# Kernel optimization log

Measured on AMD Instinct MI355X. Metric: run time of the kernel, lower is better.

The kernel has to match this reference:

```python
import jax, jax.numpy as jnp
import numpy as np

NUM_NODES = 100000
NUM_EDGES = 400000
F_IN = 16          # num_node_features
F_EDGE = 8         # num_edge_features
EMB = 16           # emb_size
NUM_GRAPHS = 256


def setup_inputs() -> dict:
    key = jax.random.key(0)
    ks = jax.random.split(key, 12)
    x = jax.random.normal(ks[0], (NUM_NODES, F_IN), dtype=jnp.float32)
    edge_index = jax.random.randint(ks[1], (2, NUM_EDGES), 0, NUM_NODES, dtype=jnp.int32)
    edge_attr = jax.random.normal(ks[2], (NUM_EDGES, F_EDGE), dtype=jnp.float32)
    batch = jnp.sort(jax.random.randint(ks[3], (NUM_NODES,), 0, NUM_GRAPHS, dtype=jnp.int32))
    s = 0.1
    # edge-network MLP: Linear(F_EDGE -> F_IN*EMB) + ReLU (torch Linear convention: W[out,in])
    nn1_w = jax.random.normal(ks[4], (F_IN * EMB, F_EDGE), dtype=jnp.float32) * s
    nn1_b = jax.random.normal(ks[5], (F_IN * EMB,), dtype=jnp.float32) * s
    # NNConv root weight (bias=False Linear) + separate bias
    root_w = jax.random.normal(ks[6], (EMB, F_IN), dtype=jnp.float32) * s
    conv_b = jax.random.normal(ks[7], (EMB,), dtype=jnp.float32) * s
    lin1_w = jax.random.normal(ks[8], (EMB, 2 * EMB), dtype=jnp.float32) * s
    lin1_b = jax.random.normal(ks[9], (EMB,), dtype=jnp.float32) * s
    lin2_w = jax.random.normal(ks[10], (1, EMB), dtype=jnp.float32) * s
    lin2_b = jax.random.normal(ks[11], (1,), dtype=jnp.float32) * s
    return {"x": x, "edge_index": edge_index, "edge_attr": edge_attr, "batch": batch,
            "nn1_w": nn1_w, "nn1_b": nn1_b, "root_w": root_w, "conv_b": conv_b,
            "lin1_w": lin1_w, "lin1_b": lin1_b, "lin2_w": lin2_w, "lin2_b": lin2_b}


def reference(x, edge_index, edge_attr, batch, nn1_w, nn1_b, root_w, conv_b,
              lin1_w, lin1_b, lin2_w, lin2_b):
    N = x.shape[0]
    src, dst = edge_index[0], edge_index[1]  # PyG: message flows src(j) -> dst(i)
    # edge network -> per-edge weight matrices [E, F_IN, EMB]
    w = jax.nn.relu(edge_attr @ nn1_w.T + nn1_b).reshape(-1, F_IN, EMB)
    # gather source features, per-edge matmul
    msg = jnp.einsum('ei,eio->eo', x[src], w)  # [E, EMB]
    # scatter-mean into target nodes
    sums = jax.ops.segment_sum(msg, dst, num_segments=N)
    cnt = jax.ops.segment_sum(jnp.ones((msg.shape[0],), msg.dtype), dst, num_segments=N)
    agg = sums / jnp.maximum(cnt, 1.0)[:, None]
    # NNConv: root transform + aggregated messages + bias, then outer ReLU
    h = jax.nn.relu(agg + x @ root_w.T + conv_b)  # [N, EMB]
    # global max pool and global mean pool per graph
    gmax = jax.ops.segment_max(h, batch, num_segments=NUM_GRAPHS)
    gsum = jax.ops.segment_sum(h, batch, num_segments=NUM_GRAPHS)
    gcnt = jax.ops.segment_sum(jnp.ones((N,), h.dtype), batch, num_segments=NUM_GRAPHS)
    gmean = gsum / jnp.maximum(gcnt, 1.0)[:, None]
    pooled = jnp.concatenate([gmax, gmean], axis=1)  # [G, 2*EMB]
    h2 = jax.nn.relu(pooled @ lin1_w.T + lin1_b)
    out = h2 @ lin2_w.T + lin2_b  # [G, 1]
    return out
```

## Files before the change

kernel.cpp:

```cpp
#include <hip/hip_runtime.h>

#define NUM_NODES 100000
#define NUM_EDGES 400000
#define F_IN 16
#define F_EDGE 8
#define EMB 16
#define NUM_GRAPHS 256

#define EDGE_TILES 5
#define EDGE_BLOCKS (NUM_EDGES / (32 * EDGE_TILES))

#define NPB 128
#define NODE_BLOCKS ((NUM_NODES + NPB - 1) / NPB)

#define WS_ZERO_FLOATS (NUM_NODES * EMB + NUM_NODES + 2 * NUM_GRAPHS * EMB + NUM_GRAPHS)

__global__ __launch_bounds__(256) void zero_kernel(float4* __restrict__ ws)
{
    const int n4 = WS_ZERO_FLOATS / 4;
    const int stride = gridDim.x * 256;
    for (int i = blockIdx.x * 256 + threadIdx.x; i < n4; i += stride)
        ws[i] = make_float4(0.f, 0.f, 0.f, 0.f);
}

__global__ __launch_bounds__(256) void edge_kernel(
    const float* __restrict__ x, const int* __restrict__ ei,
    const float* __restrict__ ea, const float* __restrict__ nn1_w,
    const float* __restrict__ nn1_b, float* __restrict__ sums,
    float* __restrict__ cnt)
{
    __shared__ float wtp[256 * 12];

    const int tid = threadIdx.x;
    const int eL  = tid >> 4;
    const int o   = tid & 15;

    #pragma unroll
    for (int t = tid; t < F_IN * EMB * F_EDGE; t += 256)
        wtp[(t >> 3) * 12 + (t & 7)] = nn1_w[t];
    wtp[tid * 12 + 8] = nn1_b[tid];
    __syncthreads();

    float br[F_IN];
    #pragma unroll
    for (int i = 0; i < F_IN; i++) br[i] = wtp[(i * 16 + o) * 12 + 8];

    for (int t = 0; t < EDGE_TILES; t++) {
        const int e0 = (blockIdx.x * EDGE_TILES + t) * 32;
        const int eA = e0 + eL;
        const int eB = e0 + 16 + eL;

        const int srcA = ei[eA];
        const int srcB = ei[eB];
        const int dstA = ei[NUM_EDGES + eA];
        const int dstB = ei[NUM_EDGES + eB];

        const float4 a00 = *(const float4*)&ea[eA * 8];
        const float4 a01 = *(const float4*)&ea[eA * 8 + 4];
        const float4 a10 = *(const float4*)&ea[eB * 8];
        const float4 a11 = *(const float4*)&ea[eB * 8 + 4];

        float xr0[F_IN], xr1[F_IN];
        #pragma unroll
        for (int r = 0; r < 4; r++) {
            const float4 v0 = *(const float4*)&x[srcA * 16 + 4 * r];
            const float4 v1 = *(const float4*)&x[srcB * 16 + 4 * r];
            xr0[4 * r + 0] = v0.x; xr0[4 * r + 1] = v0.y;
            xr0[4 * r + 2] = v0.z; xr0[4 * r + 3] = v0.w;
            xr1[4 * r + 0] = v1.x; xr1[4 * r + 1] = v1.y;
            xr1[4 * r + 2] = v1.z; xr1[4 * r + 3] = v1.w;
        }

        float acc0 = 0.f, acc1 = 0.f;
        #pragma unroll
        for (int i = 0; i < F_IN; i++) {
            const float* wr = &wtp[(i * 16 + o) * 12];
            const float4 w0 = *(const float4*)wr;
            const float4 w1 = *(const float4*)(wr + 4);
            float u = br[i];
            u = fmaf(a00.x, w0.x, u); u = fmaf(a00.y, w0.y, u);
            u = fmaf(a00.z, w0.z, u); u = fmaf(a00.w, w0.w, u);
            u = fmaf(a01.x, w1.x, u); u = fmaf(a01.y, w1.y, u);
            u = fmaf(a01.z, w1.z, u); u = fmaf(a01.w, w1.w, u);
            acc0 = fmaf(xr0[i], fmaxf(u, 0.f), acc0);
            float v = br[i];
            v = fmaf(a10.x, w0.x, v); v = fmaf(a10.y, w0.y, v);
            v = fmaf(a10.z, w0.z, v); v = fmaf(a10.w, w0.w, v);
            v = fmaf(a11.x, w1.x, v); v = fmaf(a11.y, w1.y, v);
            v = fmaf(a11.z, w1.z, v); v = fmaf(a11.w, w1.w, v);
            acc1 = fmaf(xr1[i], fmaxf(v, 0.f), acc1);
        }

        atomicAdd(&sums[dstA * 16 + o], acc0);
        atomicAdd(&sums[dstB * 16 + o], acc1);
        if (o == 0) {
            atomicAdd(&cnt[dstA], 1.f);
            atomicAdd(&cnt[dstB], 1.f);
        }
    }
}

__global__ __launch_bounds__(256) void node_kernel(
    const float* __restrict__ x, const int* __restrict__ batch,
    const float* __restrict__ root_w, const float* __restrict__ conv_b,
    const float* __restrict__ sums, const float* __restrict__ cnt,
    unsigned int* __restrict__ gmax, float* __restrict__ gsum,
    float* __restrict__ gcnt)
{
    __shared__ float rwT[256];
    __shared__ float xsh[256];
    __shared__ float ssh[256];
    __shared__ float csh[16];
    __shared__ int   bsh[16];
    __shared__ float hsh[256];

    const int tid = threadIdx.x;
    const int j   = tid >> 4;
    const int o   = tid & 15;
    const int n0  = blockIdx.x * NPB;

    rwT[(tid & 15) * 16 + (tid >> 4)] = root_w[tid];
    const float cb = conv_b[o];

    int   curg = batch[n0];
    float am = 0.f, asum = 0.f, ac = 0.f;

    for (int s0 = 0; s0 < NPB; s0 += 16) {
        const int base = n0 + s0;
        const int idx  = base * 16 + tid;
        const bool v   = (idx < NUM_NODES * 16);
        const float xv = v ? x[idx]    : 0.f;
        const float sv = v ? sums[idx] : 0.f;
        float cv = 1.f; int bv = -1;
        if (tid < 16) {
            const int n = base + tid;
            if (n < NUM_NODES) { cv = cnt[n]; bv = batch[n]; }
        }
        __syncthreads();
        xsh[tid] = xv; ssh[tid] = sv;
        if (tid < 16) { csh[tid] = cv; bsh[tid] = bv; }
        __syncthreads();

        float a = cb + ssh[j * 16 + o] / fmaxf(csh[j], 1.f);
        #pragma unroll
        for (int i = 0; i < F_IN; i++)
            a = fmaf(xsh[j * 16 + i], rwT[i * 16 + o], a);
        hsh[tid] = fmaxf(a, 0.f);
        __syncthreads();

        if (tid < 16) {
            #pragma unroll 1
            for (int jj = 0; jj < 16; jj++) {
                const int g = bsh[jj];
                if (g < 0) break;
                if (g != curg) {
                    atomicMax(&gmax[curg * 16 + o], __float_as_uint(am));
                    atomicAdd(&gsum[curg * 16 + o], asum);
                    if (o == 0) atomicAdd(&gcnt[curg], ac);
                    am = 0.f; asum = 0.f; ac = 0.f; curg = g;
                }
                const float h = hsh[jj * 16 + o];
                am = fmaxf(am, h); asum += h; ac += 1.f;
            }
        }
    }

    if (tid < 16) {
        atomicMax(&gmax[curg * 16 + o], __float_as_uint(am));
        atomicAdd(&gsum[curg * 16 + o], asum);
        if (o == 0) atomicAdd(&gcnt[curg], ac);
    }
}

__global__ __launch_bounds__(256) void head_kernel(
    const unsigned int* __restrict__ gmax, const float* __restrict__ gsum,
    const float* __restrict__ gcnt,
    const float* __restrict__ lin1_w, const float* __restrict__ lin1_b,
    const float* __restrict__ lin2_w, const float* __restrict__ lin2_b,
    float* __restrict__ out)
{
    const int g = threadIdx.x;

    float pooled[2 * EMB];
    #pragma unroll
    for (int o = 0; o < EMB; o++) pooled[o] = __uint_as_float(gmax[g * 16 + o]);
    const float c = fmaxf(gcnt[g], 1.f);
    #pragma unroll
    for (int o = 0; o < EMB; o++) pooled[EMB + o] = gsum[g * 16 + o] / c;

    float acc = lin2_b[0];
    #pragma unroll
    for (int k = 0; k < EMB; k++) {
        float a = lin1_b[k];
        #pragma unroll
        for (int cc = 0; cc < 2 * EMB; cc++)
            a = fmaf(pooled[cc], lin1_w[k * 32 + cc], a);
        acc = fmaf(fmaxf(a, 0.f), lin2_w[k], acc);
    }
    out[g] = acc;
}

extern "C" void kernel_launch(void* const* d_in, const int* in_sizes, int n_in,
                              void* d_out, int out_size, void* d_ws, size_t ws_size,
                              hipStream_t stream) {
    const float* x      = (const float*)d_in[0];
    const int*   ei     = (const int*)d_in[1];
    const float* ea     = (const float*)d_in[2];
    const int*   batch  = (const int*)d_in[3];
    const float* nn1_w  = (const float*)d_in[4];
    const float* nn1_b  = (const float*)d_in[5];
    const float* root_w = (const float*)d_in[6];
    const float* conv_b = (const float*)d_in[7];
    const float* lin1_w = (const float*)d_in[8];
    const float* lin1_b = (const float*)d_in[9];
    const float* lin2_w = (const float*)d_in[10];
    const float* lin2_b = (const float*)d_in[11];
    float* out = (float*)d_out;

    float*        sums = (float*)d_ws;
    float*        cnt  = sums + (size_t)NUM_NODES * EMB;
    unsigned int* gmax = (unsigned int*)(cnt + NUM_NODES);
    float*        gsum = (float*)(gmax + NUM_GRAPHS * EMB);
    float*        gcnt = gsum + NUM_GRAPHS * EMB;

    zero_kernel<<<1024, 256, 0, stream>>>((float4*)d_ws);
    edge_kernel<<<EDGE_BLOCKS, 256, 0, stream>>>(x, ei, ea, nn1_w, nn1_b, sums, cnt);
    node_kernel<<<NODE_BLOCKS, 256, 0, stream>>>(
        x, batch, root_w, conv_b, sums, cnt, gmax, gsum, gcnt);
    head_kernel<<<1, 256, 0, stream>>>(gmax, gsum, gcnt,
                                       lin1_w, lin1_b, lin2_w, lin2_b, out);
}
```

Before: 170.9 us.

## Process four edges per thread with grid-stride loop and vectorized index loads

Each thread now handles four consecutive edges instead of two, loading src/dst indices as int4 and edge attributes as float4s, and reusing each shared-memory weight row across four edges. The fixed-count tile loop becomes a grid-stride loop over 64-edge tiles with a fixed 2048-block grid. This cuts LDS weight reads per edge and raises memory-level parallelism. The cost is higher register pressure from holding 8 float4 attribute vectors plus gathered x values, which may lower occupancy.

```diff
diff --git a/kernel.cpp b/kernel.cpp
--- a/kernel.cpp
+++ b/kernel.cpp
@@ -7,8 +7,8 @@
 #define EMB 16
 #define NUM_GRAPHS 256
 
-#define EDGE_TILES 5
-#define EDGE_BLOCKS (NUM_EDGES / (32 * EDGE_TILES))
+#define EDGE_GRID 2048
+#define NTILES (NUM_EDGES / 64)
 
 #define NPB 128
 #define NODE_BLOCKS ((NUM_NODES + NPB - 1) / NPB)
@@ -45,57 +45,60 @@
     #pragma unroll
     for (int i = 0; i < F_IN; i++) br[i] = wtp[(i * 16 + o) * 12 + 8];
 
-    for (int t = 0; t < EDGE_TILES; t++) {
-        const int e0 = (blockIdx.x * EDGE_TILES + t) * 32;
-        const int eA = e0 + eL;
-        const int eB = e0 + 16 + eL;
-
-        const int srcA = ei[eA];
-        const int srcB = ei[eB];
-        const int dstA = ei[NUM_EDGES + eA];
-        const int dstB = ei[NUM_EDGES + eB];
-
-        const float4 a00 = *(const float4*)&ea[eA * 8];
-        const float4 a01 = *(const float4*)&ea[eA * 8 + 4];
-        const float4 a10 = *(const float4*)&ea[eB * 8];
-        const float4 a11 = *(const float4*)&ea[eB * 8 + 4];
-
-        float xr0[F_IN], xr1[F_IN];
-        #pragma unroll
-        for (int r = 0; r < 4; r++) {
-            const float4 v0 = *(const float4*)&x[srcA * 16 + 4 * r];
-            const float4 v1 = *(const float4*)&x[srcB * 16 + 4 * r];
-            xr0[4 * r + 0] = v0.x; xr0[4 * r + 1] = v0.y;
-            xr0[4 * r + 2] = v0.z; xr0[4 * r + 3] = v0.w;
-            xr1[4 * r + 0] = v1.x; xr1[4 * r + 1] = v1.y;
-            xr1[4 * r + 2] = v1.z; xr1[4 * r + 3] = v1.w;
-        }
-
-        float acc0 = 0.f, acc1 = 0.f;
-        #pragma unroll
-        for (int i = 0; i < F_IN; i++) {
-            const float* wr = &wtp[(i * 16 + o) * 12];
-            const float4 w0 = *(const float4*)wr;
-            const float4 w1 = *(const float4*)(wr + 4);
-            float u = br[i];
-            u = fmaf(a00.x, w0.x, u); u = fmaf(a00.y, w0.y, u);
-            u = fmaf(a00.z, w0.z, u); u = fmaf(a00.w, w0.w, u);
-            u = fmaf(a01.x, w1.x, u); u = fmaf(a01.y, w1.y, u);
-            u = fmaf(a01.z, w1.z, u); u = fmaf(a01.w, w1.w, u);
-            acc0 = fmaf(xr0[i], fmaxf(u, 0.f), acc0);
-            float v = br[i];
-            v = fmaf(a10.x, w0.x, v); v = fmaf(a10.y, w0.y, v);
-            v = fmaf(a10.z, w0.z, v); v = fmaf(a10.w, w0.w, v);
-            v = fmaf(a11.x, w1.x, v); v = fmaf(a11.y, w1.y, v);
-            v = fmaf(a11.z, w1.z, v); v = fmaf(a11.w, w1.w, v);
-            acc1 = fmaf(xr1[i], fmaxf(v, 0.f), acc1);
-        }
-
-        atomicAdd(&sums[dstA * 16 + o], acc0);
-        atomicAdd(&sums[dstB * 16 + o], acc1);
+    for (int t = blockIdx.x; t < NTILES; t += EDGE_GRID) {
+        const int e0 = t * 64 + eL * 4;
+
+        const int4 s4 = *(const int4*)&ei[e0];
+        const int4 d4 = *(const int4*)&ei[NUM_EDGES + e0];
+        const int src[4] = {s4.x, s4.y, s4.z, s4.w};
+        const int dst[4] = {d4.x, d4.y, d4.z, d4.w};
+
+        float4 A[8];
+        #pragma unroll
+        for (int r = 0; r < 8; r++) A[r] = *(const float4*)&ea[e0 * 8 + 4 * r];
+
+        float acc[4] = {0.f, 0.f, 0.f, 0.f};
+
+        #pragma unroll
+        for (int h = 0; h < 2; h++) {
+            float4 xa[4], xb[4];
+            #pragma unroll
+            for (int e = 0; e < 4; e++) {
+                xa[e] = *(const float4*)&x[src[e] * 16 + h * 8];
+                xb[e] = *(const float4*)&x[src[e] * 16 + h * 8 + 4];
+            }
+            #pragma unroll
+            for (int ii = 0; ii < 8; ii++) {
+                const int i = h * 8 + ii;
+                const float* wr = &wtp[(i * 16 + o) * 12];
+                const float4 w0 = *(const float4*)wr;
+                const float4 w1 = *(const float4*)(wr + 4);
+                #pragma unroll
+                for (int e = 0; e < 4; e++) {
+                    const float4 a0 = A[2 * e];
+                    const float4 a1 = A[2 * e + 1];
+                    float u = br[i];
+                    u = fmaf(a0.x, w0.x, u); u = fmaf(a0.y, w0.y, u);
+                    u = fmaf(a0.z, w0.z, u); u = fmaf(a0.w, w0.w, u);
+                    u = fmaf(a1.x, w1.x, u); u = fmaf(a1.y, w1.y, u);
+                    u = fmaf(a1.z, w1.z, u); u = fmaf(a1.w, w1.w, u);
+                    const float xv = (ii < 4)
+                        ? ((ii == 0) ? xa[e].x : (ii == 1) ? xa[e].y
+                                     : (ii == 2) ? xa[e].z : xa[e].w)
+                        : ((ii == 4) ? xb[e].x : (ii == 5) ? xb[e].y
+                                     : (ii == 6) ? xb[e].z : xb[e].w);
+                    acc[e] = fmaf(xv, fmaxf(u, 0.f), acc[e]);
+                }
+            }
+        }
+
+        #pragma unroll
+        for (int e = 0; e < 4; e++)
+            atomicAdd(&sums[dst[e] * 16 + o], acc[e]);
         if (o == 0) {
-            atomicAdd(&cnt[dstA], 1.f);
-            atomicAdd(&cnt[dstB], 1.f);
+            #pragma unroll
+            for (int e = 0; e < 4; e++)
+                atomicAdd(&cnt[dst[e]], 1.f);
         }
     }
 }
@@ -224,7 +227,7 @@
     float*        gcnt = gsum + NUM_GRAPHS * EMB;
 
     zero_kernel<<<1024, 256, 0, stream>>>((float4*)d_ws);
-    edge_kernel<<<EDGE_BLOCKS, 256, 0, stream>>>(x, ei, ea, nn1_w, nn1_b, sums, cnt);
+    edge_kernel<<<EDGE_GRID, 256, 0, stream>>>(x, ei, ea, nn1_w, nn1_b, sums, cnt);
     node_kernel<<<NODE_BLOCKS, 256, 0, stream>>>(
         x, batch, root_w, conv_b, sums, cnt, gmax, gsum, gcnt);
     head_kernel<<<1, 256, 0, stream>>>(gmax, gsum, gcnt,
```

After: 170.3 us. About the same (-0.3%).
